# Optimization experiments

Hardware: AMD Instinct MI355X
Metric: run time of the kernel (lower is better)

## Reference

```python
import jax, jax.numpy as jnp
import numpy as np

B, S, D = 2, 2048, 2048
H, KV, HD = 32, 8, 64  # num_heads, num_kv_heads, head_dim
NREP = H // KV


def rotate_half(x):
    x1, x2 = x[..., : x.shape[-1] // 2], x[..., x.shape[-1] // 2 :]
    return jnp.concatenate((-x2, x1), axis=-1)


def setup_inputs() -> dict:
    key = jax.random.key(0)
    ks = jax.random.split(key, 5)
    x = jax.random.normal(ks[0], (B, S, D), dtype=jnp.float32)
    # weights stored as [in, out] so y = x @ W (same math as nn.Linear with random init)
    Wq = jax.random.normal(ks[1], (D, D), dtype=jnp.float32) * (D ** -0.5)
    Wk = jax.random.normal(ks[2], (D, KV * HD), dtype=jnp.float32) * (D ** -0.5)
    Wv = jax.random.normal(ks[3], (D, KV * HD), dtype=jnp.float32) * (D ** -0.5)
    Wo = jax.random.normal(ks[4], (D, D), dtype=jnp.float32) * (D ** -0.5)
    # standard RoPE tables, broadcastable over [B, H, S, HD]
    inv_freq = 1.0 / (10000.0 ** (jnp.arange(0, HD, 2, dtype=jnp.float32) / HD))
    freqs = jnp.arange(S, dtype=jnp.float32)[:, None] * inv_freq[None, :]  # [S, HD/2]
    emb = jnp.concatenate((freqs, freqs), axis=-1)  # [S, HD]
    cos = jnp.cos(emb)[None, None]  # [1,1,S,HD]
    sin = jnp.sin(emb)[None, None]
    # causal mask, masked where == 0
    attention_mask = jnp.tril(jnp.ones((S, S), dtype=jnp.int32))[None, None]
    return {"x": x, "cos": cos, "sin": sin, "Wq": Wq, "Wk": Wk, "Wv": Wv,
            "Wo": Wo, "attention_mask": attention_mask}


def reference(x, cos, sin, Wq, Wk, Wv, Wo, attention_mask):
    b, s, _ = x.shape
    q = (x @ Wq).reshape(b, s, H, HD).transpose(0, 2, 1, 3)   # [B,H,S,HD]
    k = (x @ Wk).reshape(b, s, KV, HD).transpose(0, 2, 1, 3)  # [B,KV,S,HD]
    v = (x @ Wv).reshape(b, s, KV, HD).transpose(0, 2, 1, 3)  # [B,KV,S,HD]
    # RoPE (elementwise) commutes with head-repeat; apply before grouping
    q = q * cos + rotate_half(q) * sin
    k = k * cos + rotate_half(k) * sin
    # GQA head broadcast instead of repeat_interleave: group q as [B,KV,NREP,S,HD]
    qg = q.reshape(b, KV, NREP, s, HD)
    scores = jnp.einsum('bgrqd,bgkd->bgrqk', qg, k) / jnp.sqrt(jnp.float32(HD))
    scores = jnp.where(attention_mask[:, :, None] == 0, jnp.float32(-1e9), scores)
    probs = jax.nn.softmax(scores, axis=-1)
    out = jnp.einsum('bgrqk,bgkd->bgrqd', probs, v)           # [B,KV,NREP,S,HD]
    out = out.reshape(b, H, s, HD).transpose(0, 2, 1, 3).reshape(b, s, H * HD)
    return out @ Wo
```

## Files before the change

kernel.cpp:

```cpp
#include <hip/hip_runtime.h>
#include <hip/hip_bf16.h>
#include <stdint.h>

#define B_ 2
#define S_ 2048
#define D_ 2048
#define H_ 32
#define KV_ 8
#define HD_ 64
#define NQKV 3072

typedef __bf16 bf16_t;
typedef __bf16 bf16x8 __attribute__((ext_vector_type(8)));
typedef __bf16 bf16x4 __attribute__((ext_vector_type(4)));
typedef float  f32x4  __attribute__((ext_vector_type(4)));
typedef float  f32x16 __attribute__((ext_vector_type(16)));
typedef unsigned int u32;
typedef u32 u32x4 __attribute__((ext_vector_type(4)));

typedef const __attribute__((address_space(1))) uint32_t* gp1_t;
typedef __attribute__((address_space(3))) uint32_t* lp3_t;

__device__ inline void gload_lds16(const void* g, void* l) {
  __builtin_amdgcn_global_load_lds((gp1_t)(uintptr_t)g, (lp3_t)(uint32_t)(uintptr_t)l,
                                   16, 0, 0);
}

__device__ inline u32 pkbf(float a, float b) {
  union { bf16_t h[2]; u32 u; } v;
  v.h[0] = (bf16_t)a; v.h[1] = (bf16_t)b;
  return v.u;
}

__device__ inline void pl32swap(u32 &a, u32 &b) {
  asm("v_permlane32_swap_b32 %0, %1" : "+v"(a), "+v"(b));
}

__global__ void cvt_f32_bf16(const float* __restrict__ in, bf16_t* __restrict__ out, int n4) {
  int i = blockIdx.x * blockDim.x + threadIdx.x;
  if (i < n4) {
    float4 v = ((const float4*)in)[i];
    bf16x4 o;
    o[0] = (bf16_t)v.x; o[1] = (bf16_t)v.y; o[2] = (bf16_t)v.z; o[3] = (bf16_t)v.w;
    ((bf16x4*)out)[i] = o;
  }
}

__global__ void transpose_cvt_all(const float* __restrict__ Wq, const float* __restrict__ Wk,
                                  const float* __restrict__ Wv, const float* __restrict__ Wo,
                                  bf16_t* __restrict__ Wqkvt, bf16_t* __restrict__ Wot) {
  __shared__ float t[32][33];
  const int id = blockIdx.x;
  const float* in; bf16_t* out; int C, roff, bx, by;
  if (id < 4096)      { in = Wq; out = Wqkvt; C = 2048; roff = 0;    bx = id & 63;          by = id >> 6; }
  else if (id < 5120) { in = Wk; out = Wqkvt; C = 512;  roff = 2048; bx = (id - 4096) & 15; by = (id - 4096) >> 4; }
  else if (id < 6144) { in = Wv; out = Wqkvt; C = 512;  roff = 2560; bx = (id - 5120) & 15; by = (id - 5120) >> 4; }
  else                { in = Wo; out = Wot;   C = 2048; roff = 0;    bx = (id - 6144) & 63; by = (id - 6144) >> 6; }
  const int tx = threadIdx.x, ty = threadIdx.y;
  const int c0 = bx * 32, r0 = by * 32;
#pragma unroll
  for (int j = 0; j < 4; ++j)
    t[ty + j*8][tx] = in[(int64_t)(r0 + ty + j*8) * C + c0 + tx];
  __syncthreads();
#pragma unroll
  for (int j = 0; j < 4; ++j)
    out[(int64_t)(roff + c0 + ty + j*8) * 2048 + r0 + tx] = (bf16_t)t[tx][ty + j*8];
}

__global__ void v_transpose(const bf16_t* __restrict__ qkv, bf16_t* __restrict__ Vt) {
  __shared__ bf16_t t[32][34];
  const int tx = threadIdx.x, ty = threadIdx.y;
  const int c0 = blockIdx.x * 32;
  const int s0 = blockIdx.y * 32;
  const int b  = blockIdx.z;
#pragma unroll
  for (int j = 0; j < 4; ++j)
    t[ty + j*8][tx] = qkv[(int64_t)(b * S_ + s0 + ty + j*8) * NQKV + 2560 + c0 + tx];
  __syncthreads();
#pragma unroll
  for (int j = 0; j < 4; ++j)
    Vt[(int64_t)(b * 512 + c0 + ty + j*8) * S_ + s0 + tx] = t[tx][ty + j*8];
}

#define QSCALE 0.18033688011112042f
__global__ __launch_bounds__(256) void rope_scatter2(const bf16_t* __restrict__ qkv,
                                                     const float* __restrict__ cosb,
                                                     const float* __restrict__ sinb,
                                                     bf16_t* __restrict__ Q,
                                                     bf16_t* __restrict__ Kr) {
  const int row = blockIdx.x;
  const int b = row >> 11, s = row & 2047;
  const bf16_t* src = qkv + (int64_t)row * NQKV;
  const float* cs = cosb + s * HD_;
  const float* sn = sinb + s * HD_;
  const int tid = threadIdx.x;
  {
    const int c0 = tid * 8;
    const int d0 = c0 & 63, h = c0 >> 6;
    bf16x8 own = *(const bf16x8*)(src + c0);
    bf16x8 par = *(const bf16x8*)(src + (c0 ^ 32));
    const float sgn = (d0 & 32) ? 1.f : -1.f;
    bf16x8 o;
#pragma unroll
    for (int j = 0; j < 8; ++j) {
      const int d = d0 + j;
      float val = (float)own[j] * cs[d] + sgn * (float)par[j] * sn[d];
      o[j] = (bf16_t)(val * QSCALE);
    }
    *(bf16x8*)(Q + ((int64_t)(b * H_ + h) * S_ + s) * HD_ + d0) = o;
  }
  if (tid < 64) {
    const int c0 = 2048 + tid * 8;
    const int d0 = (tid * 8) & 63, kvh = tid >> 3;
    bf16x8 own = *(const bf16x8*)(src + c0);
    bf16x8 par = *(const bf16x8*)(src + (c0 ^ 32));
    const float sgn = (d0 & 32) ? 1.f : -1.f;
    bf16x8 o;
#pragma unroll
    for (int j = 0; j < 8; ++j) {
      const int d = d0 + j;
      float val = (float)own[j] * cs[d] + sgn * (float)par[j] * sn[d];
      o[j] = (bf16_t)val;
    }
    *(bf16x8*)(Kr + ((int64_t)(b * KV_ + kvh) * S_ + s) * HD_ + d0) = o;
  }
}

template <int BN, int EPI, typename OutT>
__global__ __launch_bounds__(512, 2) void gemm256(const bf16_t* __restrict__ A,
                                                  const bf16_t* __restrict__ Bt,
                                                  OutT* __restrict__ Cout,
                                                  int N, int K) {
  constexpr int NB = BN / 64;
  constexpr int LT = 4 + NB;
  constexpr int WCOLS = BN / 4;
  constexpr int NF = WCOLS / 16;

  __shared__ bf16_t As[2][256 * 64];
  __shared__ bf16_t Bs[2][BN * 64];

  const int tid = threadIdx.x;
  const int w = tid >> 6, lane = tid & 63;
  const int l15 = lane & 15, l4 = lane >> 4;
  const int wr = w >> 2, wc = w & 3;

  const int nX = gridDim.x;
  const int lin = blockIdx.y * nX + blockIdx.x;
  const int cpx = (nX * gridDim.y) >> 3;
  const int swz = (lin & 7) * cpx + (lin >> 3);
  const int bm = (swz / nX) * 256, bn = (swz % nX) * BN;

  const int rw = w * 8 + (lane >> 3);
  const int srcg = ((lane & 7) ^ ((lane >> 3) & 7)) << 3;
  const bf16_t* PA[4];
  const bf16_t* PB[NB];
#pragma unroll
  for (int L = 0; L < 4; ++L)
    PA[L] = A + (int64_t)(bm + L * 64 + rw) * K + srcg;
#pragma unroll
  for (int L = 0; L < NB; ++L)
    PB[L] = Bt + (int64_t)(bn + L * 64 + rw) * K + srcg;

  const int NK = K >> 6;
  const int xr = l15 & 7;
  const int g0 = (l4 ^ xr) << 3;
  const int g1 = ((4 + l4) ^ xr) << 3;

  f32x4 acc[8][NF] = {};

  auto stage = [&](int s, int buf, int toff) {
    if (s < 4) gload_lds16(PA[s] + toff, &As[buf][s * 4096 + w * 512]);
    else       gload_lds16(PB[s - 4] + toff, &Bs[buf][(s - 4) * 4096 + w * 512]);
  };

#pragma unroll
  for (int s = 0; s < LT; ++s) stage(s, 0, 0);
  asm volatile("s_waitcnt vmcnt(0)" ::: "memory");
  __syncthreads();

  for (int t = 0; t < NK; ++t) {
    const int p = t & 1;
    const bool more = (t + 1) < NK;
    const int toff = (t + 1) << 6;
    const bf16_t* Ab = &As[p][0];
    const bf16_t* Bb = &Bs[p][0];

    bf16x8 ball[NF][2];
#pragma unroll
    for (int nn = 0; nn < NF; ++nn) {
      const int rb = wc * WCOLS + nn * 16 + l15;
      ball[nn][0] = *(const bf16x8*)(Bb + rb * 64 + g0);
      ball[nn][1] = *(const bf16x8*)(Bb + rb * 64 + g1);
    }

#pragma unroll
    for (int mh = 0; mh < 2; ++mh) {
      if (more) {
        const int sb = mh * (LT / 2);
        const int se = (mh == 0) ? (LT / 2) : LT;
#pragma unroll
        for (int s = sb; s < se; ++s) stage(s, p ^ 1, toff);
      }
      bf16x8 af[4][2];
#pragma unroll
      for (int mm = 0; mm < 4; ++mm) {
        const int ra = wr * 128 + (mh * 4 + mm) * 16 + l15;
        af[mm][0] = *(const bf16x8*)(Ab + ra * 64 + g0);
        af[mm][1] = *(const bf16x8*)(Ab + ra * 64 + g1);
      }
      __builtin_amdgcn_s_setprio(1);
#pragma unroll
      for (int mm = 0; mm < 4; ++mm)
#pragma unroll
        for (int nn = 0; nn < NF; ++nn) {
          acc[mh*4+mm][nn] = __builtin_amdgcn_mfma_f32_16x16x32_bf16(
              af[mm][0], ball[nn][0], acc[mh*4+mm][nn], 0, 0, 0);
          acc[mh*4+mm][nn] = __builtin_amdgcn_mfma_f32_16x16x32_bf16(
              af[mm][1], ball[nn][1], acc[mh*4+mm][nn], 0, 0, 0);
        }
      __builtin_amdgcn_s_setprio(0);
    }
    if (more) {
      asm volatile("s_waitcnt vmcnt(0)" ::: "memory");
      __syncthreads();
    }
  }

#pragma unroll
  for (int m = 0; m < 8; ++m) {
    const int row = bm + wr * 128 + m * 16 + l4 * 4;
#pragma unroll
    for (int n = 0; n < NF; ++n) {
      const int col = bn + wc * WCOLS + n * 16 + l15;
#pragma unroll
      for (int r = 0; r < 4; ++r)
        Cout[(int64_t)(row + r) * N + col] = (OutT)acc[m][n][r];
    }
  }
}

#define SHIFT_ 8.0f
__global__ __launch_bounds__(256, 2) void attn9(const bf16_t* __restrict__ Q,
                                                const bf16_t* __restrict__ Kr,
                                                const bf16_t* __restrict__ Vt,
                                                bf16_t* __restrict__ AO) {
  const int bk = blockIdx.x;
  const int b = bk >> 3, kvh = bk & 7;
  const int y = blockIdx.y;
  const int q0A = y * 32, q0B = (63 - y) * 32;
  const int tid = threadIdx.x;
  const int w = tid >> 6, lane = tid & 63;
  const int l31 = lane & 31, hi = lane >> 5;
  const int h = kvh * 4 + w;

  __shared__ __align__(16) bf16_t Ks[3][64 * 64];
  __shared__ __align__(16) bf16_t Vs[3][64 * 64];

  const bf16_t* Kg = Kr + (int64_t)(b * KV_ + kvh) * S_ * HD_;
  const bf16_t* Vg = Vt + (int64_t)(b * KV_ + kvh) * HD_ * S_;

  const int rL = (w << 3) + (lane >> 3);
  const int sgr = ((lane & 7) ^ (rL & 7)) << 3;
  const bf16_t* Ksrc = Kg + (int64_t)rL * HD_ + sgr;
  const bf16_t* Vsrc = Vg + (int64_t)rL * S_ + sgr;

  const int NT = (63 - y) / 2 + 1;

  auto stage = [&](int t) {
    const int tc = (t < NT) ? t : (NT - 1);
    char* Kd = (char*)Ks + (t % 3) * 8192 + w * 1024;
    char* Vd = (char*)Vs + (t % 3) * 8192 + w * 1024;
    gload_lds16(Ksrc + (int64_t)tc * 64 * HD_, Kd);
    gload_lds16(Ksrc + (int64_t)(tc * 64 + 32) * HD_, Kd + 4096);
    gload_lds16(Vsrc + tc * 64, Vd);
    gload_lds16(Vsrc + (int64_t)32 * S_ + tc * 64, Vd + 4096);
  };

  const bf16_t* QbA = Q + ((int64_t)(b * H_ + h) * S_ + q0A) * HD_;
  const bf16_t* QbB = Q + ((int64_t)(b * H_ + h) * S_ + q0B) * HD_;
  bf16x8 qfA[4], qfB[4];
#pragma unroll
  for (int ds = 0; ds < 4; ++ds) {
    qfA[ds] = *(const bf16x8*)(QbA + l31 * HD_ + ds * 16 + hi * 8);
    qfB[ds] = *(const bf16x8*)(QbB + l31 * HD_ + ds * 16 + hi * 8);
  }

  bf16x8 onesf;
#pragma unroll
  for (int i = 0; i < 8; ++i) onesf[i] = (bf16_t)1.0f;

  f32x16 aA0 = {}, aA1 = {}, aB0 = {}, aB1 = {};
  f32x16 lA = {}, lB = {};
  const int xorb = l31 & 7;

  const f32x16 sinit = {-SHIFT_, -SHIFT_, -SHIFT_, -SHIFT_,
                        -SHIFT_, -SHIFT_, -SHIFT_, -SHIFT_,
                        -SHIFT_, -SHIFT_, -SHIFT_, -SHIFT_,
                        -SHIFT_, -SHIFT_, -SHIFT_, -SHIFT_};

  auto softmax_pack = [&](const f32x16 &sacc, bool diag,
                          bf16x8 &pf0, bf16x8 &pf1) {
    float p[16];
#pragma unroll
    for (int r = 0; r < 16; ++r) {
      float sc = sacc[r];
      if (diag) {
        int kvpos = (r & 3) + 8 * (r >> 2) + 4 * hi;
        if (kvpos > l31) sc = -1e30f;
      }
      p[r] = __builtin_amdgcn_exp2f(sc);
    }
    u32 pk[8];
#pragma unroll
    for (int i = 0; i < 8; ++i) pk[i] = pkbf(p[2*i], p[2*i+1]);
    u32 a0 = pk[0], b0 = pk[2]; pl32swap(a0, b0);
    u32 a1 = pk[1], b1 = pk[3]; pl32swap(a1, b1);
    u32 a2 = pk[4], b2 = pk[6]; pl32swap(a2, b2);
    u32 a3 = pk[5], b3 = pk[7]; pl32swap(a3, b3);
    pf0 = __builtin_bit_cast(bf16x8, (u32x4){a0, a1, b0, b1});
    pf1 = __builtin_bit_cast(bf16x8, (u32x4){a2, a3, b2, b3});
  };

  stage(0);
  stage(1);

  for (int t = 0; t < NT; ++t) {
    asm volatile("s_waitcnt vmcnt(4) lgkmcnt(0)" ::: "memory");
    asm volatile("s_barrier" ::: "memory");
    stage(t + 2);
    const char* KsB = (const char*)Ks + (t % 3) * 8192;
    const char* VsB = (const char*)Vs + (t % 3) * 8192;
#pragma unroll
    for (int sub = 0; sub < 2; ++sub) {
      const int kvbase = t * 64 + sub * 32;
      if (kvbase <= q0B) {
        const bool actA = (kvbase <= q0A);
        const char* Kbase = KsB + (sub * 32 + l31) * 128;
        bf16x8 kf[4];
#pragma unroll
        for (int ds = 0; ds < 4; ++ds)
          kf[ds] = *(const bf16x8*)(Kbase + ((((ds << 1) + hi) ^ xorb) << 4));
        f32x16 sA = sinit, sB = sinit;
        __builtin_amdgcn_s_setprio(1);
#pragma unroll
        for (int ds = 0; ds < 4; ++ds)
          sB = __builtin_amdgcn_mfma_f32_32x32x16_bf16(kf[ds], qfB[ds], sB, 0, 0, 0);
        if (actA) {
#pragma unroll
          for (int ds = 0; ds < 4; ++ds)
            sA = __builtin_amdgcn_mfma_f32_32x32x16_bf16(kf[ds], qfA[ds], sA, 0, 0, 0);
        }
        __builtin_amdgcn_s_setprio(0);
        const char* Vb0 = VsB + l31 * 128;
        const char* Vb1 = VsB + (32 + l31) * 128;
        const int c0 = (sub << 2) + hi;
        const int c1 = c0 + 2;
        bf16x8 v00 = *(const bf16x8*)(Vb0 + ((c0 ^ xorb) << 4));
        bf16x8 v01 = *(const bf16x8*)(Vb0 + ((c1 ^ xorb) << 4));
        bf16x8 v10 = *(const bf16x8*)(Vb1 + ((c0 ^ xorb) << 4));
        bf16x8 v11 = *(const bf16x8*)(Vb1 + ((c1 ^ xorb) << 4));
        bf16x8 pB0, pB1;
        softmax_pack(sB, kvbase == q0B, pB0, pB1);
        __builtin_amdgcn_s_setprio(1);
        aB0 = __builtin_amdgcn_mfma_f32_32x32x16_bf16(v00, pB0, aB0, 0, 0, 0);
        aB1 = __builtin_amdgcn_mfma_f32_32x32x16_bf16(v10, pB0, aB1, 0, 0, 0);
        aB0 = __builtin_amdgcn_mfma_f32_32x32x16_bf16(v01, pB1, aB0, 0, 0, 0);
        aB1 = __builtin_amdgcn_mfma_f32_32x32x16_bf16(v11, pB1, aB1, 0, 0, 0);
        lB  = __builtin_amdgcn_mfma_f32_32x32x16_bf16(onesf, pB0, lB, 0, 0, 0);
        lB  = __builtin_amdgcn_mfma_f32_32x32x16_bf16(onesf, pB1, lB, 0, 0, 0);
        __builtin_amdgcn_s_setprio(0);
        if (actA) {
          bf16x8 pA0, pA1;
          softmax_pack(sA, kvbase == q0A, pA0, pA1);
          __builtin_amdgcn_s_setprio(1);
          aA0 = __builtin_amdgcn_mfma_f32_32x32x16_bf16(v00, pA0, aA0, 0, 0, 0);
          aA1 = __builtin_amdgcn_mfma_f32_32x32x16_bf16(v10, pA0, aA1, 0, 0, 0);
          aA0 = __builtin_amdgcn_mfma_f32_32x32x16_bf16(v01, pA1, aA0, 0, 0, 0);
          aA1 = __builtin_amdgcn_mfma_f32_32x32x16_bf16(v11, pA1, aA1, 0, 0, 0);
          lA  = __builtin_amdgcn_mfma_f32_32x32x16_bf16(onesf, pA0, lA, 0, 0, 0);
          lA  = __builtin_amdgcn_mfma_f32_32x32x16_bf16(onesf, pA1, lA, 0, 0, 0);
          __builtin_amdgcn_s_setprio(0);
        }
      }
    }
  }

  asm volatile("s_waitcnt vmcnt(0)" ::: "memory");

  auto epi = [&](const f32x16 &a0, const f32x16 &a1, float denom, int q0) {
    const float rl = 1.f / denom;
    const int64_t row = (int64_t)(b * S_ + q0 + l31);
#pragma unroll
    for (int dt = 0; dt < 2; ++dt) {
#pragma unroll
      for (int g = 0; g < 4; ++g) {
        bf16x4 ov;
#pragma unroll
        for (int j = 0; j < 4; ++j) {
          float val = (dt ? a1[4*g + j] : a0[4*g + j]) * rl;
          ov[j] = (bf16_t)val;
        }
        const int d0 = dt * 32 + g * 8 + hi * 4;
        *(bf16x4*)(AO + row * D_ + h * HD_ + d0) = ov;
      }
    }
  };
  epi(aA0, aA1, lA[0], q0A);
  epi(aB0, aB1, lB[0], q0B);
}

extern "C" void kernel_launch(void* const* d_in, const int* in_sizes, int n_in,
                              void* d_out, int out_size, void* d_ws, size_t ws_size,
                              hipStream_t stream) {
  const float* x    = (const float*)d_in[0];
  const float* cosb = (const float*)d_in[1];
  const float* sinb = (const float*)d_in[2];
  const float* Wq   = (const float*)d_in[3];
  const float* Wk   = (const float*)d_in[4];
  const float* Wv   = (const float*)d_in[5];
  const float* Wo   = (const float*)d_in[6];
  float* out = (float*)d_out;

  bf16_t* ws = (bf16_t*)d_ws;
  size_t o = 0;
  bf16_t* xb    = ws + o; o += (size_t)4096 * 2048;
  bf16_t* Wqkvt = ws + o; o += (size_t)3072 * 2048;
  bf16_t* Wot   = ws + o; o += (size_t)2048 * 2048;
  bf16_t* qkv   = ws + o; o += (size_t)4096 * 3072;
  bf16_t* Qr    = ws + o; o += (size_t)B_ * H_ * S_ * HD_;
  bf16_t* Krb   = ws + o; o += (size_t)B_ * KV_ * S_ * HD_;
  bf16_t* Vtb   = ws + o; o += (size_t)B_ * KV_ * S_ * HD_;
  bf16_t* AO    = ws + o; o += (size_t)4096 * 2048;

  cvt_f32_bf16<<<(8388608/4 + 255)/256, 256, 0, stream>>>(x, xb, 8388608/4);
  transpose_cvt_all<<<10240, dim3(32, 8), 0, stream>>>(Wq, Wk, Wv, Wo, Wqkvt, Wot);
  gemm256<192, 2, bf16_t><<<dim3(3072/192, 4096/256), 512, 0, stream>>>(
      xb, Wqkvt, qkv, 3072, 2048);
  rope_scatter2<<<4096, 256, 0, stream>>>(qkv, cosb, sinb, Qr, Krb);
  v_transpose<<<dim3(16, 64, 2), dim3(32, 8), 0, stream>>>(qkv, Vtb);
  attn9<<<dim3(16, 32), 256, 0, stream>>>(Qr, Krb, Vtb, AO);
  gemm256<128, 0, float><<<dim3(2048/128, 4096/256), 512, 0, stream>>>(
      AO, Wot, out, 2048, 2048);
}
```

Measured before the change: 174.8 us.

## Merge prep kernels and add triple-buffered output projection GEMM

Merges the x conversion and weight transpose/convert kernels into one launch, removing a kernel boundary. Replaces the generic output-projection GEMM with a dedicated kernel that uses three LDS buffers, issues loads two tiles ahead, and waits with a partial vmcnt plus one barrier per K step instead of a full drain. This should hide global-load latency in the output GEMM at the cost of more LDS per block, which may lower occupancy.

```diff
diff --git a/kernel.cpp b/kernel.cpp
--- a/kernel.cpp
+++ b/kernel.cpp
@@ -36,26 +36,27 @@
   asm("v_permlane32_swap_b32 %0, %1" : "+v"(a), "+v"(b));
 }
 
-__global__ void cvt_f32_bf16(const float* __restrict__ in, bf16_t* __restrict__ out, int n4) {
-  int i = blockIdx.x * blockDim.x + threadIdx.x;
-  if (i < n4) {
-    float4 v = ((const float4*)in)[i];
+__global__ void prep_all(const float* __restrict__ x, bf16_t* __restrict__ xb,
+                         const float* __restrict__ Wq, const float* __restrict__ Wk,
+                         const float* __restrict__ Wv, const float* __restrict__ Wo,
+                         bf16_t* __restrict__ Wqkvt, bf16_t* __restrict__ Wot) {
+  const int id = blockIdx.x;
+  const int tid = threadIdx.y * 32 + threadIdx.x;
+  if (id < 8192) {
+    const int i = id * 256 + tid;
+    float4 v = ((const float4*)x)[i];
     bf16x4 o;
     o[0] = (bf16_t)v.x; o[1] = (bf16_t)v.y; o[2] = (bf16_t)v.z; o[3] = (bf16_t)v.w;
-    ((bf16x4*)out)[i] = o;
-  }
-}
-
-__global__ void transpose_cvt_all(const float* __restrict__ Wq, const float* __restrict__ Wk,
-                                  const float* __restrict__ Wv, const float* __restrict__ Wo,
-                                  bf16_t* __restrict__ Wqkvt, bf16_t* __restrict__ Wot) {
+    ((bf16x4*)xb)[i] = o;
+    return;
+  }
   __shared__ float t[32][33];
-  const int id = blockIdx.x;
+  const int wid = id - 8192;
   const float* in; bf16_t* out; int C, roff, bx, by;
-  if (id < 4096)      { in = Wq; out = Wqkvt; C = 2048; roff = 0;    bx = id & 63;          by = id >> 6; }
-  else if (id < 5120) { in = Wk; out = Wqkvt; C = 512;  roff = 2048; bx = (id - 4096) & 15; by = (id - 4096) >> 4; }
-  else if (id < 6144) { in = Wv; out = Wqkvt; C = 512;  roff = 2560; bx = (id - 5120) & 15; by = (id - 5120) >> 4; }
-  else                { in = Wo; out = Wot;   C = 2048; roff = 0;    bx = (id - 6144) & 63; by = (id - 6144) >> 6; }
+  if (wid < 4096)      { in = Wq; out = Wqkvt; C = 2048; roff = 0;    bx = wid & 63;          by = wid >> 6; }
+  else if (wid < 5120) { in = Wk; out = Wqkvt; C = 512;  roff = 2048; bx = (wid - 4096) & 15; by = (wid - 4096) >> 4; }
+  else if (wid < 6144) { in = Wv; out = Wqkvt; C = 512;  roff = 2560; bx = (wid - 5120) & 15; by = (wid - 5120) >> 4; }
+  else                 { in = Wo; out = Wot;   C = 2048; roff = 0;    bx = (wid - 6144) & 63; by = (wid - 6144) >> 6; }
   const int tx = threadIdx.x, ty = threadIdx.y;
   const int c0 = bx * 32, r0 = by * 32;
 #pragma unroll
@@ -235,6 +236,109 @@
 #pragma unroll
       for (int r = 0; r < 4; ++r)
         Cout[(int64_t)(row + r) * N + col] = (OutT)acc[m][n][r];
+    }
+  }
+}
+
+__global__ __launch_bounds__(512, 2) void gemm_out3(const bf16_t* __restrict__ A,
+                                                    const bf16_t* __restrict__ Bt,
+                                                    float* __restrict__ Cout,
+                                                    int N, int K) {
+  constexpr int BN = 128, NB = 2, LT = 6, WCOLS = 32, NF = 2;
+
+  __shared__ bf16_t As[3][256 * 64];
+  __shared__ bf16_t Bs[3][BN * 64];
+
+  const int tid = threadIdx.x;
+  const int w = tid >> 6, lane = tid & 63;
+  const int l15 = lane & 15, l4 = lane >> 4;
+  const int wr = w >> 2, wc = w & 3;
+
+  const int nX = gridDim.x;
+  const int lin = blockIdx.y * nX + blockIdx.x;
+  const int cpx = (nX * gridDim.y) >> 3;
+  const int swz = (lin & 7) * cpx + (lin >> 3);
+  const int bm = (swz / nX) * 256, bn = (swz % nX) * BN;
+
+  const int rw = w * 8 + (lane >> 3);
+  const int srcg = ((lane & 7) ^ ((lane >> 3) & 7)) << 3;
+  const bf16_t* PA[4];
+  const bf16_t* PB[NB];
+#pragma unroll
+  for (int L = 0; L < 4; ++L)
+    PA[L] = A + (int64_t)(bm + L * 64 + rw) * K + srcg;
+#pragma unroll
+  for (int L = 0; L < NB; ++L)
+    PB[L] = Bt + (int64_t)(bn + L * 64 + rw) * K + srcg;
+
+  const int NK = K >> 6;
+  const int xr = l15 & 7;
+  const int g0 = (l4 ^ xr) << 3;
+  const int g1 = ((4 + l4) ^ xr) << 3;
+
+  f32x4 acc[8][NF] = {};
+
+  auto stage = [&](int tsrc, int buf) {
+    const int tc = (tsrc < NK) ? tsrc : (NK - 1);
+    const int toff = tc << 6;
+#pragma unroll
+    for (int s = 0; s < 4; ++s)
+      gload_lds16(PA[s] + toff, &As[buf][s * 4096 + w * 512]);
+#pragma unroll
+    for (int s = 0; s < NB; ++s)
+      gload_lds16(PB[s] + toff, &Bs[buf][s * 4096 + w * 512]);
+  };
+
+  stage(0, 0);
+  stage(1, 1);
+
+  for (int t = 0; t < NK; ++t) {
+    asm volatile("s_waitcnt vmcnt(6)" ::: "memory");
+    asm volatile("s_barrier" ::: "memory");
+    stage(t + 2, (t + 2) % 3);
+    const bf16_t* Ab = &As[t % 3][0];
+    const bf16_t* Bb = &Bs[t % 3][0];
+
+    bf16x8 ball[NF][2];
+#pragma unroll
+    for (int nn = 0; nn < NF; ++nn) {
+      const int rb = wc * WCOLS + nn * 16 + l15;
+      ball[nn][0] = *(const bf16x8*)(Bb + rb * 64 + g0);
+      ball[nn][1] = *(const bf16x8*)(Bb + rb * 64 + g1);
+    }
+#pragma unroll
+    for (int mh = 0; mh < 2; ++mh) {
+      bf16x8 af[4][2];
+#pragma unroll
+      for (int mm = 0; mm < 4; ++mm) {
+        const int ra = wr * 128 + (mh * 4 + mm) * 16 + l15;
+        af[mm][0] = *(const bf16x8*)(Ab + ra * 64 + g0);
+        af[mm][1] = *(const bf16x8*)(Ab + ra * 64 + g1);
+      }
+      __builtin_amdgcn_s_setprio(1);
+#pragma unroll
+      for (int mm = 0; mm < 4; ++mm)
+#pragma unroll
+        for (int nn = 0; nn < NF; ++nn) {
+          acc[mh*4+mm][nn] = __builtin_amdgcn_mfma_f32_16x16x32_bf16(
+              af[mm][0], ball[nn][0], acc[mh*4+mm][nn], 0, 0, 0);
+          acc[mh*4+mm][nn] = __builtin_amdgcn_mfma_f32_16x16x32_bf16(
+              af[mm][1], ball[nn][1], acc[mh*4+mm][nn], 0, 0, 0);
+        }
+      __builtin_amdgcn_s_setprio(0);
+    }
+  }
+  asm volatile("s_waitcnt vmcnt(0)" ::: "memory");
+
+#pragma unroll
+  for (int m = 0; m < 8; ++m) {
+    const int row = bm + wr * 128 + m * 16 + l4 * 4;
+#pragma unroll
+    for (int n = 0; n < NF; ++n) {
+      const int col = bn + wc * WCOLS + n * 16 + l15;
+#pragma unroll
+      for (int r = 0; r < 4; ++r)
+        Cout[(int64_t)(row + r) * N + col] = acc[m][n][r];
     }
   }
 }
@@ -432,13 +536,11 @@
   bf16_t* Vtb   = ws + o; o += (size_t)B_ * KV_ * S_ * HD_;
   bf16_t* AO    = ws + o; o += (size_t)4096 * 2048;
 
-  cvt_f32_bf16<<<(8388608/4 + 255)/256, 256, 0, stream>>>(x, xb, 8388608/4);
-  transpose_cvt_all<<<10240, dim3(32, 8), 0, stream>>>(Wq, Wk, Wv, Wo, Wqkvt, Wot);
+  prep_all<<<18432, dim3(32, 8), 0, stream>>>(x, xb, Wq, Wk, Wv, Wo, Wqkvt, Wot);
   gemm256<192, 2, bf16_t><<<dim3(3072/192, 4096/256), 512, 0, stream>>>(
       xb, Wqkvt, qkv, 3072, 2048);
   rope_scatter2<<<4096, 256, 0, stream>>>(qkv, cosb, sinb, Qr, Krb);
   v_transpose<<<dim3(16, 64, 2), dim3(32, 8), 0, stream>>>(qkv, Vtb);
   attn9<<<dim3(16, 32), 256, 0, stream>>>(Qr, Krb, Vtb, AO);
-  gemm256<128, 0, float><<<dim3(2048/128, 4096/256), 512, 0, stream>>>(
-      AO, Wot, out, 2048, 2048);
-}
+  gemm_out3<<<dim3(2048/128, 4096/256), 512, 0, stream>>>(AO, Wot, out, 2048, 2048);
+}
```

Result: no change. 173.4 us (-0.8%).

## Merge prep and scatter kernels; process full 64-key tile per attention step

Applied to the files above, without the earlier changes.

Merges the x conversion and weight transpose into one launch, and merges RoPE scatter with the V transpose into another, removing two kernel launches and their gaps. The attention inner loop now handles both 32-key halves of a 64-key tile together, issuing independent QK MFMAs for both halves back to back and loading all V fragments at once. The aim is better MFMA interleaving and less per-subtile branching, at the cost of more live registers, which may pressure occupancy at two blocks per CU.

```diff
diff --git a/kernel.cpp b/kernel.cpp
--- a/kernel.cpp
+++ b/kernel.cpp
@@ -36,26 +36,27 @@
   asm("v_permlane32_swap_b32 %0, %1" : "+v"(a), "+v"(b));
 }
 
-__global__ void cvt_f32_bf16(const float* __restrict__ in, bf16_t* __restrict__ out, int n4) {
-  int i = blockIdx.x * blockDim.x + threadIdx.x;
-  if (i < n4) {
-    float4 v = ((const float4*)in)[i];
+__global__ void prep_all(const float* __restrict__ x, bf16_t* __restrict__ xb,
+                         const float* __restrict__ Wq, const float* __restrict__ Wk,
+                         const float* __restrict__ Wv, const float* __restrict__ Wo,
+                         bf16_t* __restrict__ Wqkvt, bf16_t* __restrict__ Wot) {
+  const int id = blockIdx.x;
+  const int tid = threadIdx.y * 32 + threadIdx.x;
+  if (id < 8192) {
+    const int i = id * 256 + tid;
+    float4 v = ((const float4*)x)[i];
     bf16x4 o;
     o[0] = (bf16_t)v.x; o[1] = (bf16_t)v.y; o[2] = (bf16_t)v.z; o[3] = (bf16_t)v.w;
-    ((bf16x4*)out)[i] = o;
+    ((bf16x4*)xb)[i] = o;
+    return;
   }
-}
-
-__global__ void transpose_cvt_all(const float* __restrict__ Wq, const float* __restrict__ Wk,
-                                  const float* __restrict__ Wv, const float* __restrict__ Wo,
-                                  bf16_t* __restrict__ Wqkvt, bf16_t* __restrict__ Wot) {
   __shared__ float t[32][33];
-  const int id = blockIdx.x;
+  const int wid = id - 8192;
   const float* in; bf16_t* out; int C, roff, bx, by;
-  if (id < 4096)      { in = Wq; out = Wqkvt; C = 2048; roff = 0;    bx = id & 63;          by = id >> 6; }
-  else if (id < 5120) { in = Wk; out = Wqkvt; C = 512;  roff = 2048; bx = (id - 4096) & 15; by = (id - 4096) >> 4; }
-  else if (id < 6144) { in = Wv; out = Wqkvt; C = 512;  roff = 2560; bx = (id - 5120) & 15; by = (id - 5120) >> 4; }
-  else                { in = Wo; out = Wot;   C = 2048; roff = 0;    bx = (id - 6144) & 63; by = (id - 6144) >> 6; }
+  if (wid < 4096)      { in = Wq; out = Wqkvt; C = 2048; roff = 0;    bx = wid & 63;          by = wid >> 6; }
+  else if (wid < 5120) { in = Wk; out = Wqkvt; C = 512;  roff = 2048; bx = (wid - 4096) & 15; by = (wid - 4096) >> 4; }
+  else if (wid < 6144) { in = Wv; out = Wqkvt; C = 512;  roff = 2560; bx = (wid - 5120) & 15; by = (wid - 5120) >> 4; }
+  else                 { in = Wo; out = Wot;   C = 2048; roff = 0;    bx = (wid - 6144) & 63; by = (wid - 6144) >> 6; }
   const int tx = threadIdx.x, ty = threadIdx.y;
   const int c0 = bx * 32, r0 = by * 32;
 #pragma unroll
@@ -67,12 +68,59 @@
     out[(int64_t)(roff + c0 + ty + j*8) * 2048 + r0 + tx] = (bf16_t)t[tx][ty + j*8];
 }
 
-__global__ void v_transpose(const bf16_t* __restrict__ qkv, bf16_t* __restrict__ Vt) {
+#define QSCALE 0.18033688011112042f
+__global__ __launch_bounds__(256) void scatter_all(const bf16_t* __restrict__ qkv,
+                                                   const float* __restrict__ cosb,
+                                                   const float* __restrict__ sinb,
+                                                   bf16_t* __restrict__ Q,
+                                                   bf16_t* __restrict__ Kr,
+                                                   bf16_t* __restrict__ Vt) {
+  const int id = blockIdx.x;
+  const int tid = threadIdx.x;
+  if (id < 4096) {
+    const int row = id;
+    const int b = row >> 11, s = row & 2047;
+    const bf16_t* src = qkv + (int64_t)row * NQKV;
+    const float* cs = cosb + s * HD_;
+    const float* sn = sinb + s * HD_;
+    {
+      const int c0 = tid * 8;
+      const int d0 = c0 & 63, h = c0 >> 6;
+      bf16x8 own = *(const bf16x8*)(src + c0);
+      bf16x8 par = *(const bf16x8*)(src + (c0 ^ 32));
+      const float sgn = (d0 & 32) ? 1.f : -1.f;
+      bf16x8 o;
+#pragma unroll
+      for (int j = 0; j < 8; ++j) {
+        const int d = d0 + j;
+        float val = (float)own[j] * cs[d] + sgn * (float)par[j] * sn[d];
+        o[j] = (bf16_t)(val * QSCALE);
+      }
+      *(bf16x8*)(Q + ((int64_t)(b * H_ + h) * S_ + s) * HD_ + d0) = o;
+    }
+    if (tid < 64) {
+      const int c0 = 2048 + tid * 8;
+      const int d0 = (tid * 8) & 63, kvh = tid >> 3;
+      bf16x8 own = *(const bf16x8*)(src + c0);
+      bf16x8 par = *(const bf16x8*)(src + (c0 ^ 32));
+      const float sgn = (d0 & 32) ? 1.f : -1.f;
+      bf16x8 o;
+#pragma unroll
+      for (int j = 0; j < 8; ++j) {
+        const int d = d0 + j;
+        float val = (float)own[j] * cs[d] + sgn * (float)par[j] * sn[d];
+        o[j] = (bf16_t)val;
+      }
+      *(bf16x8*)(Kr + ((int64_t)(b * KV_ + kvh) * S_ + s) * HD_ + d0) = o;
+    }
+    return;
+  }
   __shared__ bf16_t t[32][34];
-  const int tx = threadIdx.x, ty = threadIdx.y;
-  const int c0 = blockIdx.x * 32;
-  const int s0 = blockIdx.y * 32;
-  const int b  = blockIdx.z;
+  const int wid = id - 4096;
+  const int c0 = (wid & 15) * 32;
+  const int s0 = ((wid >> 4) & 63) * 32;
+  const int b  = wid >> 10;
+  const int tx = tid & 31, ty = tid >> 5;
 #pragma unroll
   for (int j = 0; j < 4; ++j)
     t[ty + j*8][tx] = qkv[(int64_t)(b * S_ + s0 + ty + j*8) * NQKV + 2560 + c0 + tx];
@@ -80,50 +128,6 @@
 #pragma unroll
   for (int j = 0; j < 4; ++j)
     Vt[(int64_t)(b * 512 + c0 + ty + j*8) * S_ + s0 + tx] = t[tx][ty + j*8];
-}
-
-#define QSCALE 0.18033688011112042f
-__global__ __launch_bounds__(256) void rope_scatter2(const bf16_t* __restrict__ qkv,
-                                                     const float* __restrict__ cosb,
-                                                     const float* __restrict__ sinb,
-                                                     bf16_t* __restrict__ Q,
-                                                     bf16_t* __restrict__ Kr) {
-  const int row = blockIdx.x;
-  const int b = row >> 11, s = row & 2047;
-  const bf16_t* src = qkv + (int64_t)row * NQKV;
-  const float* cs = cosb + s * HD_;
-  const float* sn = sinb + s * HD_;
-  const int tid = threadIdx.x;
-  {
-    const int c0 = tid * 8;
-    const int d0 = c0 & 63, h = c0 >> 6;
-    bf16x8 own = *(const bf16x8*)(src + c0);
-    bf16x8 par = *(const bf16x8*)(src + (c0 ^ 32));
-    const float sgn = (d0 & 32) ? 1.f : -1.f;
-    bf16x8 o;
-#pragma unroll
-    for (int j = 0; j < 8; ++j) {
-      const int d = d0 + j;
-      float val = (float)own[j] * cs[d] + sgn * (float)par[j] * sn[d];
-      o[j] = (bf16_t)(val * QSCALE);
-    }
-    *(bf16x8*)(Q + ((int64_t)(b * H_ + h) * S_ + s) * HD_ + d0) = o;
-  }
-  if (tid < 64) {
-    const int c0 = 2048 + tid * 8;
-    const int d0 = (tid * 8) & 63, kvh = tid >> 3;
-    bf16x8 own = *(const bf16x8*)(src + c0);
-    bf16x8 par = *(const bf16x8*)(src + (c0 ^ 32));
-    const float sgn = (d0 & 32) ? 1.f : -1.f;
-    bf16x8 o;
-#pragma unroll
-    for (int j = 0; j < 8; ++j) {
-      const int d = d0 + j;
-      float val = (float)own[j] * cs[d] + sgn * (float)par[j] * sn[d];
-      o[j] = (bf16_t)val;
-    }
-    *(bf16x8*)(Kr + ((int64_t)(b * KV_ + kvh) * S_ + s) * HD_ + d0) = o;
-  }
 }
 
 template <int BN, int EPI, typename OutT>
@@ -240,10 +244,10 @@
 }
 
 #define SHIFT_ 8.0f
-__global__ __launch_bounds__(256, 2) void attn9(const bf16_t* __restrict__ Q,
-                                                const bf16_t* __restrict__ Kr,
-                                                const bf16_t* __restrict__ Vt,
-                                                bf16_t* __restrict__ AO) {
+__global__ __launch_bounds__(256, 2) void attn10(const bf16_t* __restrict__ Q,
+                                                 const bf16_t* __restrict__ Kr,
+                                                 const bf16_t* __restrict__ Vt,
+                                                 bf16_t* __restrict__ AO) {
   const int bk = blockIdx.x;
   const int b = bk >> 3, kvh = bk & 7;
   const int y = blockIdx.y;
@@ -330,58 +334,113 @@
     stage(t + 2);
     const char* KsB = (const char*)Ks + (t % 3) * 8192;
     const char* VsB = (const char*)Vs + (t % 3) * 8192;
-#pragma unroll
-    for (int sub = 0; sub < 2; ++sub) {
-      const int kvbase = t * 64 + sub * 32;
-      if (kvbase <= q0B) {
-        const bool actA = (kvbase <= q0A);
-        const char* Kbase = KsB + (sub * 32 + l31) * 128;
-        bf16x8 kf[4];
+    const int kv0 = t * 64;
+    const char* Vb0 = VsB + l31 * 128;
+    const char* Vb1 = VsB + (32 + l31) * 128;
+    auto vld = [&](const char* base, int c) {
+      return *(const bf16x8*)(base + ((c ^ xorb) << 4));
+    };
+
+    if (kv0 + 32 <= q0B) {
+      const bool actA0 = (kv0 <= q0A), actA1 = (kv0 + 32 <= q0A);
+      const bool dB1 = (kv0 + 32 == q0B);
+      const bool dA0 = (kv0 == q0A), dA1 = (kv0 + 32 == q0A);
+      const char* Kb0 = KsB + l31 * 128;
+      const char* Kb1 = KsB + (32 + l31) * 128;
+      bf16x8 kf0[4], kf1[4];
+#pragma unroll
+      for (int ds = 0; ds < 4; ++ds) {
+        kf0[ds] = *(const bf16x8*)(Kb0 + ((((ds << 1) + hi) ^ xorb) << 4));
+        kf1[ds] = *(const bf16x8*)(Kb1 + ((((ds << 1) + hi) ^ xorb) << 4));
+      }
+      f32x16 s0 = sinit, s1 = sinit;
+      __builtin_amdgcn_s_setprio(1);
+#pragma unroll
+      for (int ds = 0; ds < 4; ++ds) {
+        s0 = __builtin_amdgcn_mfma_f32_32x32x16_bf16(kf0[ds], qfB[ds], s0, 0, 0, 0);
+        s1 = __builtin_amdgcn_mfma_f32_32x32x16_bf16(kf1[ds], qfB[ds], s1, 0, 0, 0);
+      }
+      __builtin_amdgcn_s_setprio(0);
+      bf16x8 pB00, pB01, pB10, pB11;
+      softmax_pack(s0, false, pB00, pB01);
+      softmax_pack(s1, dB1, pB10, pB11);
+      f32x16 t0 = sinit, t1 = sinit;
+      __builtin_amdgcn_s_setprio(1);
+      if (actA0) {
 #pragma unroll
         for (int ds = 0; ds < 4; ++ds)
-          kf[ds] = *(const bf16x8*)(Kbase + ((((ds << 1) + hi) ^ xorb) << 4));
-        f32x16 sA = sinit, sB = sinit;
+          t0 = __builtin_amdgcn_mfma_f32_32x32x16_bf16(kf0[ds], qfA[ds], t0, 0, 0, 0);
+      }
+      if (actA1) {
+#pragma unroll
+        for (int ds = 0; ds < 4; ++ds)
+          t1 = __builtin_amdgcn_mfma_f32_32x32x16_bf16(kf1[ds], qfA[ds], t1, 0, 0, 0);
+      }
+      bf16x8 v00 = vld(Vb0, hi),     v01 = vld(Vb0, 2 + hi);
+      bf16x8 v10 = vld(Vb1, hi),     v11 = vld(Vb1, 2 + hi);
+      bf16x8 w00 = vld(Vb0, 4 + hi), w01 = vld(Vb0, 6 + hi);
+      bf16x8 w10 = vld(Vb1, 4 + hi), w11 = vld(Vb1, 6 + hi);
+      aB0 = __builtin_amdgcn_mfma_f32_32x32x16_bf16(v00, pB00, aB0, 0, 0, 0);
+      aB1 = __builtin_amdgcn_mfma_f32_32x32x16_bf16(v10, pB00, aB1, 0, 0, 0);
+      aB0 = __builtin_amdgcn_mfma_f32_32x32x16_bf16(v01, pB01, aB0, 0, 0, 0);
+      aB1 = __builtin_amdgcn_mfma_f32_32x32x16_bf16(v11, pB01, aB1, 0, 0, 0);
+      aB0 = __builtin_amdgcn_mfma_f32_32x32x16_bf16(w00, pB10, aB0, 0, 0, 0);
+      aB1 = __builtin_amdgcn_mfma_f32_32x32x16_bf16(w10, pB10, aB1, 0, 0, 0);
+      aB0 = __builtin_amdgcn_mfma_f32_32x32x16_bf16(w01, pB11, aB0, 0, 0, 0);
+      aB1 = __builtin_amdgcn_mfma_f32_32x32x16_bf16(w11, pB11, aB1, 0, 0, 0);
+      lB  = __builtin_amdgcn_mfma_f32_32x32x16_bf16(onesf, pB00, lB, 0, 0, 0);
+      lB  = __builtin_amdgcn_mfma_f32_32x32x16_bf16(onesf, pB01, lB, 0, 0, 0);
+      lB  = __builtin_amdgcn_mfma_f32_32x32x16_bf16(onesf, pB10, lB, 0, 0, 0);
+      lB  = __builtin_amdgcn_mfma_f32_32x32x16_bf16(onesf, pB11, lB, 0, 0, 0);
+      __builtin_amdgcn_s_setprio(0);
+      if (actA0) {
+        bf16x8 pA0, pA1;
+        softmax_pack(t0, dA0, pA0, pA1);
         __builtin_amdgcn_s_setprio(1);
-#pragma unroll
-        for (int ds = 0; ds < 4; ++ds)
-          sB = __builtin_amdgcn_mfma_f32_32x32x16_bf16(kf[ds], qfB[ds], sB, 0, 0, 0);
-        if (actA) {
-#pragma unroll
-          for (int ds = 0; ds < 4; ++ds)
-            sA = __builtin_amdgcn_mfma_f32_32x32x16_bf16(kf[ds], qfA[ds], sA, 0, 0, 0);
-        }
+        aA0 = __builtin_amdgcn_mfma_f32_32x32x16_bf16(v00, pA0, aA0, 0, 0, 0);
+        aA1 = __builtin_amdgcn_mfma_f32_32x32x16_bf16(v10, pA0, aA1, 0, 0, 0);
+        aA0 = __builtin_amdgcn_mfma_f32_32x32x16_bf16(v01, pA1, aA0, 0, 0, 0);
+        aA1 = __builtin_amdgcn_mfma_f32_32x32x16_bf16(v11, pA1, aA1, 0, 0, 0);
+        lA  = __builtin_amdgcn_mfma_f32_32x32x16_bf16(onesf, pA0, lA, 0, 0, 0);
+        lA  = __builtin_amdgcn_mfma_f32_32x32x16_bf16(onesf, pA1, lA, 0, 0, 0);
         __builtin_amdgcn_s_setprio(0);
-        const char* Vb0 = VsB + l31 * 128;
-        const char* Vb1 = VsB + (32 + l31) * 128;
-        const int c0 = (sub << 2) + hi;
-        const int c1 = c0 + 2;
-        bf16x8 v00 = *(const bf16x8*)(Vb0 + ((c0 ^ xorb) << 4));
-        bf16x8 v01 = *(const bf16x8*)(Vb0 + ((c1 ^ xorb) << 4));
-        bf16x8 v10 = *(const bf16x8*)(Vb1 + ((c0 ^ xorb) << 4));
-        bf16x8 v11 = *(const bf16x8*)(Vb1 + ((c1 ^ xorb) << 4));
-        bf16x8 pB0, pB1;
-        softmax_pack(sB, kvbase == q0B, pB0, pB1);
+      }
+      if (actA1) {
+        bf16x8 pA0, pA1;
+        softmax_pack(t1, dA1, pA0, pA1);
         __builtin_amdgcn_s_setprio(1);
-        aB0 = __builtin_amdgcn_mfma_f32_32x32x16_bf16(v00, pB0, aB0, 0, 0, 0);
-        aB1 = __builtin_amdgcn_mfma_f32_32x32x16_bf16(v10, pB0, aB1, 0, 0, 0);
-        aB0 = __builtin_amdgcn_mfma_f32_32x32x16_bf16(v01, pB1, aB0, 0, 0, 0);
-        aB1 = __builtin_amdgcn_mfma_f32_32x32x16_bf16(v11, pB1, aB1, 0, 0, 0);
-        lB  = __builtin_amdgcn_mfma_f32_32x32x16_bf16(onesf, pB0, lB, 0, 0, 0);
-        lB  = __builtin_amdgcn_mfma_f32_32x32x16_bf16(onesf, pB1, lB, 0, 0, 0);
+        aA0 = __builtin_amdgcn_mfma_f32_32x32x16_bf16(w00, pA0, aA0, 0, 0, 0);
+        aA1 = __builtin_amdgcn_mfma_f32_32x32x16_bf16(w10, pA0, aA1, 0, 0, 0);
+        aA0 = __builtin_amdgcn_mfma_f32_32x32x16_bf16(w01, pA1, aA0, 0, 0, 0);
+        aA1 = __builtin_amdgcn_mfma_f32_32x32x16_bf16(w11, pA1, aA1, 0, 0, 0);
+        lA  = __builtin_amdgcn_mfma_f32_32x32x16_bf16(onesf, pA0, lA, 0, 0, 0);
+        lA  = __builtin_amdgcn_mfma_f32_32x32x16_bf16(onesf, pA1, lA, 0, 0, 0);
         __builtin_amdgcn_s_setprio(0);
-        if (actA) {
-          bf16x8 pA0, pA1;
-          softmax_pack(sA, kvbase == q0A, pA0, pA1);
-          __builtin_amdgcn_s_setprio(1);
-          aA0 = __builtin_amdgcn_mfma_f32_32x32x16_bf16(v00, pA0, aA0, 0, 0, 0);
-          aA1 = __builtin_amdgcn_mfma_f32_32x32x16_bf16(v10, pA0, aA1, 0, 0, 0);
-          aA0 = __builtin_amdgcn_mfma_f32_32x32x16_bf16(v01, pA1, aA0, 0, 0, 0);
-          aA1 = __builtin_amdgcn_mfma_f32_32x32x16_bf16(v11, pA1, aA1, 0, 0, 0);
-          lA  = __builtin_amdgcn_mfma_f32_32x32x16_bf16(onesf, pA0, lA, 0, 0, 0);
-          lA  = __builtin_amdgcn_mfma_f32_32x32x16_bf16(onesf, pA1, lA, 0, 0, 0);
-          __builtin_amdgcn_s_setprio(0);
-        }
-      }
+      }
+    } else if (kv0 <= q0B) {
+      const char* Kb0 = KsB + l31 * 128;
+      bf16x8 kf0[4];
+#pragma unroll
+      for (int ds = 0; ds < 4; ++ds)
+        kf0[ds] = *(const bf16x8*)(Kb0 + ((((ds << 1) + hi) ^ xorb) << 4));
+      f32x16 s0 = sinit;
+      __builtin_amdgcn_s_setprio(1);
+#pragma unroll
+      for (int ds = 0; ds < 4; ++ds)
+        s0 = __builtin_amdgcn_mfma_f32_32x32x16_bf16(kf0[ds], qfB[ds], s0, 0, 0, 0);
+      __builtin_amdgcn_s_setprio(0);
+      bf16x8 pB0, pB1;
+      softmax_pack(s0, kv0 == q0B, pB0, pB1);
+      bf16x8 v00 = vld(Vb0, hi), v01 = vld(Vb0, 2 + hi);
+      bf16x8 v10 = vld(Vb1, hi), v11 = vld(Vb1, 2 + hi);
+      __builtin_amdgcn_s_setprio(1);
+      aB0 = __builtin_amdgcn_mfma_f32_32x32x16_bf16(v00, pB0, aB0, 0, 0, 0);
+      aB1 = __builtin_amdgcn_mfma_f32_32x32x16_bf16(v10, pB0, aB1, 0, 0, 0);
+      aB0 = __builtin_amdgcn_mfma_f32_32x32x16_bf16(v01, pB1, aB0, 0, 0, 0);
+      aB1 = __builtin_amdgcn_mfma_f32_32x32x16_bf16(v11, pB1, aB1, 0, 0, 0);
+      lB  = __builtin_amdgcn_mfma_f32_32x32x16_bf16(onesf, pB0, lB, 0, 0, 0);
+      lB  = __builtin_amdgcn_mfma_f32_32x32x16_bf16(onesf, pB1, lB, 0, 0, 0);
+      __builtin_amdgcn_s_setprio(0);
     }
   }
 
@@ -432,13 +491,11 @@
   bf16_t* Vtb   = ws + o; o += (size_t)B_ * KV_ * S_ * HD_;
   bf16_t* AO    = ws + o; o += (size_t)4096 * 2048;
 
-  cvt_f32_bf16<<<(8388608/4 + 255)/256, 256, 0, stream>>>(x, xb, 8388608/4);
-  transpose_cvt_all<<<10240, dim3(32, 8), 0, stream>>>(Wq, Wk, Wv, Wo, Wqkvt, Wot);
+  prep_all<<<18432, dim3(32, 8), 0, stream>>>(x, xb, Wq, Wk, Wv, Wo, Wqkvt, Wot);
   gemm256<192, 2, bf16_t><<<dim3(3072/192, 4096/256), 512, 0, stream>>>(
       xb, Wqkvt, qkv, 3072, 2048);
-  rope_scatter2<<<4096, 256, 0, stream>>>(qkv, cosb, sinb, Qr, Krb);
-  v_transpose<<<dim3(16, 64, 2), dim3(32, 8), 0, stream>>>(qkv, Vtb);
-  attn9<<<dim3(16, 32), 256, 0, stream>>>(Qr, Krb, Vtb, AO);
+  scatter_all<<<6144, 256, 0, stream>>>(qkv, cosb, sinb, Qr, Krb, Vtb);
+  attn10<<<dim3(16, 32), 256, 0, stream>>>(Qr, Krb, Vtb, AO);
   gemm256<128, 0, float><<<dim3(2048/128, 4096/256), 512, 0, stream>>>(
       AO, Wot, out, 2048, 2048);
 }
```

Measured after the change: 172.2 us. Within noise of the previous version (-1.5%).
